# Kernel tuning notes

Measured on AMD Instinct MI355X. Metric: run time of the kernel, lower is better.

Reference implementation:

```python
import jax, jax.numpy as jnp
import numpy as np


def setup_inputs() -> dict:
    key = jax.random.key(0)
    k1, k2, k3 = jax.random.split(key, 3)
    B, C_IN, C_OUT, K, S = 2, 16, 16, 3, 24
    x = jax.random.normal(k1, (B, C_IN, S, S, S, S), dtype=jnp.float32)
    # weight in canonical [out, in, kh, kw, kd, kt] layout (the torch module's
    # pre-permutation is a storage detail; the math is a standard 4D cross-correlation)
    w = jax.random.normal(k2, (C_OUT, C_IN, K, K, K, K), dtype=jnp.float32) * 0.05
    b = jax.random.normal(k3, (C_OUT,), dtype=jnp.float32) * 0.05
    return {"x": x, "w": w, "b": b}


def reference(x, w, b):
    # 4D convolution with 'same' padding (pad = k//2 in every spatial dim),
    # stride 1, no dilation — exactly what the looped conv4d() computes.
    dn = jax.lax.conv_dimension_numbers(x.shape, w.shape, ("NCHWDT", "OIHWDT", "NCHWDT"))
    out = jax.lax.conv_general_dilated(
        x, w,
        window_strides=(1, 1, 1, 1),
        padding="SAME",
        dimension_numbers=dn,
    )
    return out + b[None, :, None, None, None, None]
```

## Files before the change

kernel.cpp:

```cpp
#include <hip/hip_runtime.h>

typedef __attribute__((ext_vector_type(8))) short bfrag;
typedef __attribute__((ext_vector_type(4))) float f32x4;

#define XS4 331776
#define XS3 13824
#define XS2 576

#define WS_ZERO   86016
#define WS_XS     86080
#define XS_HALF_B 5308416
#define WS_NEED   42553408ull
#define NSITE     1260
#define NSITE_PAD 1280
#define LDS_LO    20480

__global__ void wsplit_kernel(const float* __restrict__ w,
                              unsigned int* __restrict__ ws) {
    int e = blockIdx.x * 256 + threadIdx.x;
    int ci2 = e & 3;
    int co  = (e >> 2) & 15;
    int t84 = e >> 6;
    int tau = t84 % 84;
    int cs  = t84 / 84;
    int ch  = cs >> 1;
    int s   = cs & 1;

    unsigned int outv = 0u;
    if (tau < 81) {
        unsigned int half[2];
#pragma unroll
        for (int q = 0; q < 2; ++q) {
            int ci = ch * 8 + ci2 * 2 + q;
            union { float f; unsigned u; } v;
            v.f = w[(co * 16 + ci) * 81 + tau];
            unsigned hi = v.u & 0xFFFF0000u;
            union { unsigned u; float f; } hv; hv.u = hi;
            union { float f; unsigned u; } rv; rv.f = v.f - hv.f;
            unsigned lo = rv.u & 0xFFFF0000u;
            half[q] = (s == 0) ? hi : lo;
        }
        outv = (half[0] >> 16) | (half[1] & 0xFFFF0000u);
    }
    ws[e] = outv;
    if (e < 16) ws[(WS_ZERO / 4) + e] = 0u;
}

__global__ void xsplit_kernel(const float* __restrict__ x,
                              unsigned short* __restrict__ xs) {
    int s4 = blockIdx.x * 256 + threadIdx.x;
    int bc = blockIdx.y;
    const float* xp = x + (size_t)(bc * 8) * XS4 + s4;
    unsigned hib[8], lob[8];
#pragma unroll
    for (int c = 0; c < 8; ++c) {
        union { float f; unsigned u; } v;
        v.f = xp[(size_t)c * XS4];
        unsigned hi = v.u & 0xFFFF0000u;
        union { unsigned u; float f; } hv; hv.u = hi;
        union { float f; unsigned u; } rv; rv.f = v.f - hv.f;
        hib[c] = hi;
        lob[c] = rv.u & 0xFFFF0000u;
    }
    uint4 ph, pl;
    ph.x = (hib[0] >> 16) | (hib[1] & 0xFFFF0000u);
    ph.y = (hib[2] >> 16) | (hib[3] & 0xFFFF0000u);
    ph.z = (hib[4] >> 16) | (hib[5] & 0xFFFF0000u);
    ph.w = (hib[6] >> 16) | (hib[7] & 0xFFFF0000u);
    pl.x = (lob[0] >> 16) | (lob[1] & 0xFFFF0000u);
    pl.y = (lob[2] >> 16) | (lob[3] & 0xFFFF0000u);
    pl.z = (lob[4] >> 16) | (lob[5] & 0xFFFF0000u);
    pl.w = (lob[6] >> 16) | (lob[7] & 0xFFFF0000u);
    *(uint4*)(xs + ((size_t)(bc * 2 + 0) * XS4 + s4) * 8) = ph;
    *(uint4*)(xs + ((size_t)(bc * 2 + 1) * XS4 + s4) * 8) = pl;
}

__global__ __launch_bounds__(192, 3)
void conv4d_mfma_v2(const unsigned short* __restrict__ xs,
                    const unsigned short* __restrict__ wfrag,
                    const char* __restrict__ zptr,
                    const float* __restrict__ bias,
                    float* __restrict__ out) {
    __shared__ __align__(16) unsigned short xhl[2 * NSITE_PAD * 8];

    const int tid  = threadIdx.x;
    const int l    = tid & 63;
    const int wv   = tid >> 6;

    int bid = blockIdx.x;
    const int b    = bid / 3456;
    int r          = bid % 3456;
    const int h    = r / 144;
    r              = r % 144;
    const int w0   = r / 6;
    const int seg  = r % 6;
    const int dbase = (seg >> 1) * 8, tbase = (seg & 1) * 12;

    const int i_  = l & 15;
    const int tl4 = l >> 4;
    const int d_i = i_ >> 2;
    const int t_i = i_ & 3;
    const int co  = l & 15;

    const int mt0 = wv * 2, mt1 = wv * 2 + 1;
    const int dq0 = mt0 / 3, tq0 = mt0 % 3;
    const int dq1 = mt1 / 3, tq1 = mt1 % 3;
    const int la0 = dq0 * 896 + tq0 * 64 + d_i * 224 + t_i * 16;
    const int la1 = dq1 * 896 + tq1 * 64 + d_i * 224 + t_i * 16;

    int aoffs[21];
#pragma unroll
    for (int g = 0; g < 21; ++g) {
        int tau  = 4 * g + tl4;
        int teff = tau > 80 ? 80 : tau;
        int p    = teff / 9;
        int r9   = teff - p * 9;
        int kd   = r9 / 3;
        int kt   = r9 - kd * 3;
        aoffs[g] = p * 2240 + kd * 224 + kt * 16;
    }

    f32x4 acc0 = {0.f, 0.f, 0.f, 0.f};
    f32x4 acc1 = {0.f, 0.f, 0.f, 0.f};

    const char* xbase = (const char*)&xhl[0];
    const char* xsb   = (const char*)xs;
    const char* wB    = (const char*)wfrag + tl4 * 256 + co * 16;

    for (int ch = 0; ch < 2; ++ch) {
        __syncthreads();

        const unsigned base16 = (unsigned)((b * 2 + ch) * 2) * (unsigned)(XS4 * 16);

        for (int k = 0; k < 7; ++k) {
            int idx0 = k * 192 + wv * 64;
            if (idx0 < NSITE_PAD) {
                int idx = idx0 + l;
                int p  = idx / 140;
                int rr = idx - p * 140;
                int dd = rr / 14;
                int tt = rr - dd * 14;
                int hh = h  + p / 3 - 1;
                int ww = w0 + p % 3 - 1;
                int dp = dbase + dd - 1;
                int tp = tbase + tt - 1;
                bool valid = ((unsigned)hh < 24u) && ((unsigned)ww < 24u) &&
                             ((unsigned)dp < 24u) && ((unsigned)tp < 24u) &&
                             (idx < NSITE);
                const char* gh = zptr;
                const char* gl = zptr;
                if (valid) {
                    unsigned off = base16 +
                        (unsigned)(hh * XS3 + ww * XS2 + dp * 24 + tp) * 16u;
                    gh = xsb + off;
                    gl = gh + XS_HALF_B;
                }
                char* lp = (char*)&xhl[0] + idx * 16;
                __builtin_amdgcn_global_load_lds(
                    (const __attribute__((address_space(1))) void*)gh,
                    (__attribute__((address_space(3))) void*)lp, 16, 0, 0);
                __builtin_amdgcn_global_load_lds(
                    (const __attribute__((address_space(1))) void*)gl,
                    (__attribute__((address_space(3))) void*)(lp + LDS_LO), 16, 0, 0);
            }
        }
        __syncthreads();

        const char* pw = wB + ch * 43008;

#pragma unroll
        for (int g = 0; g < 21; ++g) {
            bfrag whf = *(const bfrag*)(pw + g * 1024);
            bfrag wlf = *(const bfrag*)(pw + g * 1024 + 21504);

            const char* ax = xbase + aoffs[g];
            bfrag xh0 = *(const bfrag*)(ax + la0);
            bfrag xl0 = *(const bfrag*)(ax + la0 + LDS_LO);
            bfrag xh1 = *(const bfrag*)(ax + la1);
            bfrag xl1 = *(const bfrag*)(ax + la1 + LDS_LO);

            __builtin_amdgcn_s_setprio(1);
            acc0 = __builtin_amdgcn_mfma_f32_16x16x32_bf16(xh0, whf, acc0, 0, 0, 0);
            acc1 = __builtin_amdgcn_mfma_f32_16x16x32_bf16(xh1, whf, acc1, 0, 0, 0);
            acc0 = __builtin_amdgcn_mfma_f32_16x16x32_bf16(xh0, wlf, acc0, 0, 0, 0);
            acc1 = __builtin_amdgcn_mfma_f32_16x16x32_bf16(xh1, wlf, acc1, 0, 0, 0);
            acc0 = __builtin_amdgcn_mfma_f32_16x16x32_bf16(xl0, whf, acc0, 0, 0, 0);
            acc1 = __builtin_amdgcn_mfma_f32_16x16x32_bf16(xl1, whf, acc1, 0, 0, 0);
            __builtin_amdgcn_s_setprio(0);
        }
    }

    const float bv = bias[co];
    const int ob = (b * 16 + co) * XS4 + h * XS3 + w0 * XS2;
    {
        int d = dbase + dq0 * 4 + tl4;
        int t = tbase + tq0 * 4;
        float4 v;
        v.x = acc0[0] + bv; v.y = acc0[1] + bv;
        v.z = acc0[2] + bv; v.w = acc0[3] + bv;
        *(float4*)&out[ob + d * 24 + t] = v;
    }
    {
        int d = dbase + dq1 * 4 + tl4;
        int t = tbase + tq1 * 4;
        float4 v;
        v.x = acc1[0] + bv; v.y = acc1[1] + bv;
        v.z = acc1[2] + bv; v.w = acc1[3] + bv;
        *(float4*)&out[ob + d * 24 + t] = v;
    }
}

__global__ __launch_bounds__(192, 3)
void conv4d_mfma_v1(const float* __restrict__ x,
                    const unsigned short* __restrict__ wfrag,
                    const float* __restrict__ bias,
                    float* __restrict__ out) {
    __shared__ __align__(16) unsigned short xhl[2][1260][8];

    const int tid = threadIdx.x;
    const int l   = tid & 63;

    int bid = blockIdx.x;
    const int b    = bid / 3456;
    int r          = bid % 3456;
    const int h    = r / 144;
    r              = r % 144;
    const int w0   = r / 6;
    const int seg  = r % 6;
    const int dbase = (seg >> 1) * 8, tbase = (seg & 1) * 12;

    const int i_  = l & 15;
    const int tl4 = l >> 4;
    const int d_i = i_ >> 2;
    const int t_i = i_ & 3;
    const int co  = l & 15;

    const int wv  = tid >> 6;
    const int mt0 = wv * 2, mt1 = wv * 2 + 1;
    const int dq0 = mt0 / 3, tq0 = mt0 % 3;
    const int dq1 = mt1 / 3, tq1 = mt1 % 3;
    const int la0 = dq0 * 896 + tq0 * 64 + d_i * 224 + t_i * 16;
    const int la1 = dq1 * 896 + tq1 * 64 + d_i * 224 + t_i * 16;

    f32x4 acc0 = {0.f, 0.f, 0.f, 0.f};
    f32x4 acc1 = {0.f, 0.f, 0.f, 0.f};

    const char* xbase = (const char*)&xhl[0][0][0];
    const char* wB    = (const char*)wfrag + tl4 * 256 + co * 16;

    for (int ch = 0; ch < 2; ++ch) {
        __syncthreads();
        for (int k = 0; k < 7; ++k) {
            int idx = tid + k * 192;
            if (idx < 1260) {
                int p  = idx / 140;
                int rr = idx - p * 140;
                int dd = rr / 14;
                int tt = rr - dd * 14;
                int hh = h  + p / 3 - 1;
                int ww = w0 + p % 3 - 1;
                int dp = dbase + dd - 1;
                int tp = tbase + tt - 1;
                unsigned hib[8], lob[8];
                bool valid = ((unsigned)hh < 24u) && ((unsigned)ww < 24u) &&
                             ((unsigned)dp < 24u) && ((unsigned)tp < 24u);
                if (valid) {
                    int g = b * (16 * XS4) + (ch * 8) * XS4
                          + hh * XS3 + ww * XS2 + dp * 24 + tp;
#pragma unroll
                    for (int c = 0; c < 8; ++c) {
                        union { float f; unsigned u; } v;
                        v.f = x[g + c * XS4];
                        unsigned hi = v.u & 0xFFFF0000u;
                        union { unsigned u; float f; } hv; hv.u = hi;
                        union { float f; unsigned u; } rv2; rv2.f = v.f - hv.f;
                        hib[c] = hi;
                        lob[c] = rv2.u & 0xFFFF0000u;
                    }
                } else {
#pragma unroll
                    for (int c = 0; c < 8; ++c) { hib[c] = 0u; lob[c] = 0u; }
                }
                uint4 ph, pl;
                ph.x = (hib[0] >> 16) | (hib[1] & 0xFFFF0000u);
                ph.y = (hib[2] >> 16) | (hib[3] & 0xFFFF0000u);
                ph.z = (hib[4] >> 16) | (hib[5] & 0xFFFF0000u);
                ph.w = (hib[6] >> 16) | (hib[7] & 0xFFFF0000u);
                pl.x = (lob[0] >> 16) | (lob[1] & 0xFFFF0000u);
                pl.y = (lob[2] >> 16) | (lob[3] & 0xFFFF0000u);
                pl.z = (lob[4] >> 16) | (lob[5] & 0xFFFF0000u);
                pl.w = (lob[6] >> 16) | (lob[7] & 0xFFFF0000u);
                *(uint4*)((char*)&xhl[0][0][0] + idx * 16)         = ph;
                *(uint4*)((char*)&xhl[0][0][0] + 20160 + idx * 16) = pl;
            }
        }
        __syncthreads();

        const char* pw = wB + ch * 43008;
#pragma unroll
        for (int g = 0; g < 21; ++g) {
            bfrag whf = *(const bfrag*)(pw + g * 1024);
            bfrag wlf = *(const bfrag*)(pw + g * 1024 + 21504);

            int tau  = 4 * g + tl4;
            int teff = tau > 80 ? 80 : tau;
            int p    = teff / 9;
            int r9   = teff - p * 9;
            int kd   = r9 / 3;
            int kt   = r9 - kd * 3;
            int aoff = p * 2240 + kd * 224 + kt * 16;

            const char* ax = xbase + aoff;
            bfrag xh0 = *(const bfrag*)(ax + la0);
            bfrag xl0 = *(const bfrag*)(ax + la0 + 20160);
            bfrag xh1 = *(const bfrag*)(ax + la1);
            bfrag xl1 = *(const bfrag*)(ax + la1 + 20160);

            acc0 = __builtin_amdgcn_mfma_f32_16x16x32_bf16(xh0, whf, acc0, 0, 0, 0);
            acc1 = __builtin_amdgcn_mfma_f32_16x16x32_bf16(xh1, whf, acc1, 0, 0, 0);
            acc0 = __builtin_amdgcn_mfma_f32_16x16x32_bf16(xh0, wlf, acc0, 0, 0, 0);
            acc1 = __builtin_amdgcn_mfma_f32_16x16x32_bf16(xh1, wlf, acc1, 0, 0, 0);
            acc0 = __builtin_amdgcn_mfma_f32_16x16x32_bf16(xl0, whf, acc0, 0, 0, 0);
            acc1 = __builtin_amdgcn_mfma_f32_16x16x32_bf16(xl1, whf, acc1, 0, 0, 0);
        }
    }

    const float bv = bias[co];
    const int ob = (b * 16 + co) * XS4 + h * XS3 + w0 * XS2;
    {
        int d = dbase + dq0 * 4 + tl4;
        int t = tbase + tq0 * 4;
        float4 v;
        v.x = acc0[0] + bv; v.y = acc0[1] + bv;
        v.z = acc0[2] + bv; v.w = acc0[3] + bv;
        *(float4*)&out[ob + d * 24 + t] = v;
    }
    {
        int d = dbase + dq1 * 4 + tl4;
        int t = tbase + tq1 * 4;
        float4 v;
        v.x = acc1[0] + bv; v.y = acc1[1] + bv;
        v.z = acc1[2] + bv; v.w = acc1[3] + bv;
        *(float4*)&out[ob + d * 24 + t] = v;
    }
}

extern "C" void kernel_launch(void* const* d_in, const int* in_sizes, int n_in,
                              void* d_out, int out_size, void* d_ws, size_t ws_size,
                              hipStream_t stream) {
    const float* x    = (const float*)d_in[0];
    const float* w    = (const float*)d_in[1];
    const float* bias = (const float*)d_in[2];
    float* out        = (float*)d_out;
    char* ws          = (char*)d_ws;
    unsigned* wfrag   = (unsigned*)ws;

    wsplit_kernel<<<84, 256, 0, stream>>>(w, wfrag);

    if (ws_size >= WS_NEED) {
        unsigned short* xs = (unsigned short*)(ws + WS_XS);
        xsplit_kernel<<<dim3(1296, 4), 256, 0, stream>>>(x, xs);
        conv4d_mfma_v2<<<6912, 192, 0, stream>>>(
            xs, (const unsigned short*)wfrag, ws + WS_ZERO, bias, out);
    } else {
        conv4d_mfma_v1<<<6912, 192, 0, stream>>>(
            x, (const unsigned short*)wfrag, bias, out);
    }
}
```

Before: 231.2 us.

## Merge weight and input split kernels; transpose LDS tile to t-major order

Combines the weight-split and input-split preprocessing into a single launch, removing one kernel launch and its gap. It also changes the LDS staging layout of the input halo tile from d-major (14 t per d) to t-major (10 d per t), updating the A-fragment offsets to match. The new layout changes the LDS bank access pattern and the global gather order for the 16-byte loads. That could reduce bank conflicts, or it could hurt global load coalescing because consecutive lanes now step along d instead of t.

```diff
diff --git a/kernel.cpp b/kernel.cpp
--- a/kernel.cpp
+++ b/kernel.cpp
@@ -15,68 +15,71 @@
 #define NSITE_PAD 1280
 #define LDS_LO    20480
 
-__global__ void wsplit_kernel(const float* __restrict__ w,
-                              unsigned int* __restrict__ ws) {
-    int e = blockIdx.x * 256 + threadIdx.x;
-    int ci2 = e & 3;
-    int co  = (e >> 2) & 15;
-    int t84 = e >> 6;
-    int tau = t84 % 84;
-    int cs  = t84 / 84;
-    int ch  = cs >> 1;
-    int s   = cs & 1;
-
-    unsigned int outv = 0u;
-    if (tau < 81) {
-        unsigned int half[2];
-#pragma unroll
-        for (int q = 0; q < 2; ++q) {
-            int ci = ch * 8 + ci2 * 2 + q;
+__global__ void presplit_kernel(const float* __restrict__ x,
+                                const float* __restrict__ w,
+                                unsigned int* __restrict__ ws,
+                                unsigned short* __restrict__ xs) {
+    int bid = blockIdx.x;
+    int tid = threadIdx.x;
+    if (bid < 84) {
+        int e = bid * 256 + tid;
+        int ci2 = e & 3;
+        int co  = (e >> 2) & 15;
+        int t84 = e >> 6;
+        int tau = t84 % 84;
+        int cs  = t84 / 84;
+        int ch  = cs >> 1;
+        int s   = cs & 1;
+        unsigned int outv = 0u;
+        if (tau < 81) {
+            unsigned int half[2];
+#pragma unroll
+            for (int q = 0; q < 2; ++q) {
+                int ci = ch * 8 + ci2 * 2 + q;
+                union { float f; unsigned u; } v;
+                v.f = w[(co * 16 + ci) * 81 + tau];
+                unsigned hi = v.u & 0xFFFF0000u;
+                union { unsigned u; float f; } hv; hv.u = hi;
+                union { float f; unsigned u; } rv; rv.f = v.f - hv.f;
+                unsigned lo = rv.u & 0xFFFF0000u;
+                half[q] = (s == 0) ? hi : lo;
+            }
+            outv = (half[0] >> 16) | (half[1] & 0xFFFF0000u);
+        }
+        ws[e] = outv;
+        if (e < 16) ws[(WS_ZERO / 4) + e] = 0u;
+    } else {
+        int xb = bid - 84;
+        int s4 = (xb % 1296) * 256 + tid;
+        int bc = xb / 1296;
+        const float* xp = x + (size_t)(bc * 8) * XS4 + s4;
+        unsigned hib[8], lob[8];
+#pragma unroll
+        for (int c = 0; c < 8; ++c) {
             union { float f; unsigned u; } v;
-            v.f = w[(co * 16 + ci) * 81 + tau];
+            v.f = xp[(size_t)c * XS4];
             unsigned hi = v.u & 0xFFFF0000u;
             union { unsigned u; float f; } hv; hv.u = hi;
             union { float f; unsigned u; } rv; rv.f = v.f - hv.f;
-            unsigned lo = rv.u & 0xFFFF0000u;
-            half[q] = (s == 0) ? hi : lo;
-        }
-        outv = (half[0] >> 16) | (half[1] & 0xFFFF0000u);
-    }
-    ws[e] = outv;
-    if (e < 16) ws[(WS_ZERO / 4) + e] = 0u;
+            hib[c] = hi;
+            lob[c] = rv.u & 0xFFFF0000u;
+        }
+        uint4 ph, pl;
+        ph.x = (hib[0] >> 16) | (hib[1] & 0xFFFF0000u);
+        ph.y = (hib[2] >> 16) | (hib[3] & 0xFFFF0000u);
+        ph.z = (hib[4] >> 16) | (hib[5] & 0xFFFF0000u);
+        ph.w = (hib[6] >> 16) | (hib[7] & 0xFFFF0000u);
+        pl.x = (lob[0] >> 16) | (lob[1] & 0xFFFF0000u);
+        pl.y = (lob[2] >> 16) | (lob[3] & 0xFFFF0000u);
+        pl.z = (lob[4] >> 16) | (lob[5] & 0xFFFF0000u);
+        pl.w = (lob[6] >> 16) | (lob[7] & 0xFFFF0000u);
+        *(uint4*)(xs + ((size_t)(bc * 2 + 0) * XS4 + s4) * 8) = ph;
+        *(uint4*)(xs + ((size_t)(bc * 2 + 1) * XS4 + s4) * 8) = pl;
+    }
 }
 
-__global__ void xsplit_kernel(const float* __restrict__ x,
-                              unsigned short* __restrict__ xs) {
-    int s4 = blockIdx.x * 256 + threadIdx.x;
-    int bc = blockIdx.y;
-    const float* xp = x + (size_t)(bc * 8) * XS4 + s4;
-    unsigned hib[8], lob[8];
-#pragma unroll
-    for (int c = 0; c < 8; ++c) {
-        union { float f; unsigned u; } v;
-        v.f = xp[(size_t)c * XS4];
-        unsigned hi = v.u & 0xFFFF0000u;
-        union { unsigned u; float f; } hv; hv.u = hi;
-        union { float f; unsigned u; } rv; rv.f = v.f - hv.f;
-        hib[c] = hi;
-        lob[c] = rv.u & 0xFFFF0000u;
-    }
-    uint4 ph, pl;
-    ph.x = (hib[0] >> 16) | (hib[1] & 0xFFFF0000u);
-    ph.y = (hib[2] >> 16) | (hib[3] & 0xFFFF0000u);
-    ph.z = (hib[4] >> 16) | (hib[5] & 0xFFFF0000u);
-    ph.w = (hib[6] >> 16) | (hib[7] & 0xFFFF0000u);
-    pl.x = (lob[0] >> 16) | (lob[1] & 0xFFFF0000u);
-    pl.y = (lob[2] >> 16) | (lob[3] & 0xFFFF0000u);
-    pl.z = (lob[4] >> 16) | (lob[5] & 0xFFFF0000u);
-    pl.w = (lob[6] >> 16) | (lob[7] & 0xFFFF0000u);
-    *(uint4*)(xs + ((size_t)(bc * 2 + 0) * XS4 + s4) * 8) = ph;
-    *(uint4*)(xs + ((size_t)(bc * 2 + 1) * XS4 + s4) * 8) = pl;
-}
-
 __global__ __launch_bounds__(192, 3)
-void conv4d_mfma_v2(const unsigned short* __restrict__ xs,
+void conv4d_mfma_v3(const unsigned short* __restrict__ xs,
                     const unsigned short* __restrict__ wfrag,
                     const char* __restrict__ zptr,
                     const float* __restrict__ bias,
@@ -105,8 +108,8 @@
     const int mt0 = wv * 2, mt1 = wv * 2 + 1;
     const int dq0 = mt0 / 3, tq0 = mt0 % 3;
     const int dq1 = mt1 / 3, tq1 = mt1 % 3;
-    const int la0 = dq0 * 896 + tq0 * 64 + d_i * 224 + t_i * 16;
-    const int la1 = dq1 * 896 + tq1 * 64 + d_i * 224 + t_i * 16;
+    const int la0 = tq0 * 640 + t_i * 160 + dq0 * 64 + d_i * 16;
+    const int la1 = tq1 * 640 + t_i * 160 + dq1 * 64 + d_i * 16;
 
     int aoffs[21];
 #pragma unroll
@@ -117,7 +120,7 @@
         int r9   = teff - p * 9;
         int kd   = r9 / 3;
         int kt   = r9 - kd * 3;
-        aoffs[g] = p * 2240 + kd * 224 + kt * 16;
+        aoffs[g] = p * 2240 + kt * 160 + kd * 16;
     }
 
     f32x4 acc0 = {0.f, 0.f, 0.f, 0.f};
@@ -138,8 +141,8 @@
                 int idx = idx0 + l;
                 int p  = idx / 140;
                 int rr = idx - p * 140;
-                int dd = rr / 14;
-                int tt = rr - dd * 14;
+                int tt = rr / 10;
+                int dd = rr - tt * 10;
                 int hh = h  + p / 3 - 1;
                 int ww = w0 + p % 3 - 1;
                 int dp = dbase + dd - 1;
@@ -210,6 +213,35 @@
     }
 }
 
+__global__ void wsplit_kernel(const float* __restrict__ w,
+                              unsigned int* __restrict__ ws) {
+    int e = blockIdx.x * 256 + threadIdx.x;
+    int ci2 = e & 3;
+    int co  = (e >> 2) & 15;
+    int t84 = e >> 6;
+    int tau = t84 % 84;
+    int cs  = t84 / 84;
+    int ch  = cs >> 1;
+    int s   = cs & 1;
+    unsigned int outv = 0u;
+    if (tau < 81) {
+        unsigned int half[2];
+#pragma unroll
+        for (int q = 0; q < 2; ++q) {
+            int ci = ch * 8 + ci2 * 2 + q;
+            union { float f; unsigned u; } v;
+            v.f = w[(co * 16 + ci) * 81 + tau];
+            unsigned hi = v.u & 0xFFFF0000u;
+            union { unsigned u; float f; } hv; hv.u = hi;
+            union { float f; unsigned u; } rv; rv.f = v.f - hv.f;
+            unsigned lo = rv.u & 0xFFFF0000u;
+            half[q] = (s == 0) ? hi : lo;
+        }
+        outv = (half[0] >> 16) | (half[1] & 0xFFFF0000u);
+    }
+    ws[e] = outv;
+}
+
 __global__ __launch_bounds__(192, 3)
 void conv4d_mfma_v1(const float* __restrict__ x,
                     const unsigned short* __restrict__ wfrag,
@@ -355,14 +387,13 @@
     char* ws          = (char*)d_ws;
     unsigned* wfrag   = (unsigned*)ws;
 
-    wsplit_kernel<<<84, 256, 0, stream>>>(w, wfrag);
-
     if (ws_size >= WS_NEED) {
-        unsigned short* xs = (unsigned short*)(ws + WS_XS);
-        xsplit_kernel<<<dim3(1296, 4), 256, 0, stream>>>(x, xs);
-        conv4d_mfma_v2<<<6912, 192, 0, stream>>>(
-            xs, (const unsigned short*)wfrag, ws + WS_ZERO, bias, out);
+        unsigned short* xsq = (unsigned short*)(ws + WS_XS);
+        presplit_kernel<<<84 + 5184, 256, 0, stream>>>(x, w, wfrag, xsq);
+        conv4d_mfma_v3<<<6912, 192, 0, stream>>>(
+            xsq, (const unsigned short*)wfrag, ws + WS_ZERO, bias, out);
     } else {
+        wsplit_kernel<<<84, 256, 0, stream>>>(w, wfrag);
         conv4d_mfma_v1<<<6912, 192, 0, stream>>>(
             x, (const unsigned short*)wfrag, bias, out);
     }
```

New measurement: 238.8 us. +3.3%, slower.
